# Kernel optimization log

Measured on AMD Instinct MI355X. Metric: run time of the kernel, lower is better.

Reference implementation:

```python
import jax, jax.numpy as jnp
import numpy as np

D_IN = 1024
D_OUT = 1024
B, S = 4, 4096


def setup_inputs() -> dict:
    key = jax.random.key(0)
    ks = jax.random.split(key, 7)
    scale = 1.0 / np.sqrt(D_IN)
    return {
        "x": jax.random.normal(ks[0], (B, S, D_IN), dtype=jnp.float32),
        "Wq": jax.random.uniform(ks[1], (D_IN, D_OUT), jnp.float32, -scale, scale),
        "bq": jax.random.uniform(ks[2], (D_OUT,), jnp.float32, -scale, scale),
        "Wk": jax.random.uniform(ks[3], (D_IN, D_OUT), jnp.float32, -scale, scale),
        "bk": jax.random.uniform(ks[4], (D_OUT,), jnp.float32, -scale, scale),
        "Wv": jax.random.uniform(ks[5], (D_IN, D_OUT), jnp.float32, -scale, scale),
        "bv": jax.random.uniform(ks[6], (D_OUT,), jnp.float32, -scale, scale),
    }


def reference(x, Wq, bq, Wk, bk, Wv, bv):
    # x: [B,S,d_in]
    q = jnp.einsum("bsd,de->bse", x, Wq) + bq  # [B,S,d_out]
    k = jnp.einsum("bsd,de->bse", x, Wk) + bk
    v = jnp.einsum("bsd,de->bse", x, Wv) + bv
    scores = jnp.einsum("bqe,bke->bqk", q, k) / jnp.sqrt(jnp.float32(D_OUT))  # [B,S,S]
    attn = jax.nn.softmax(scores, axis=2)
    return jnp.einsum("bqk,bke->bqe", attn, v)  # [B,S,d_out]
```

## Files before the change

### kernel.cpp

```cpp
#include <hip/hip_runtime.h>
#include <hip/hip_bf16.h>
#include <cstdint>

#define SEQ 4096
#define NB 4
#define DIM 1024
#define MTOT (NB * SEQ)
constexpr size_t EL = (size_t)MTOT * DIM;

using u16x8  = __attribute__((ext_vector_type(8))) unsigned short;
using bf16x8 = __attribute__((ext_vector_type(8))) __bf16;
using f32x4  = __attribute__((ext_vector_type(4))) float;

__device__ __forceinline__ unsigned short f2bf(float f) {
  return __builtin_bit_cast(unsigned short, __float2bfloat16(f));
}

__device__ __forceinline__ void gload16(const unsigned short* g, unsigned short* l) {
  __builtin_amdgcn_global_load_lds(
      (const __attribute__((address_space(1))) unsigned int*)g,
      (__attribute__((address_space(3))) unsigned int*)l, 16, 0, 0);
}
__device__ __forceinline__ void stage_half(const unsigned short* gsrc, size_t ld,
                                           unsigned short* ldst) {
  gload16(gsrc, ldst);
  gload16(gsrc + 64 * ld, ldst + 64 * 64);
}

#define BAR()   __builtin_amdgcn_s_barrier()
#define FENCE() asm volatile("" ::: "memory")

__global__ __launch_bounds__(256) void prep(const float* __restrict__ x,
                                            unsigned short* __restrict__ xb,
                                            const float* __restrict__ bq,
                                            const float* __restrict__ bk,
                                            const float* __restrict__ bv,
                                            float* __restrict__ bc,
                                            float* __restrict__ l) {
  const size_t gid = (size_t)blockIdx.x * 256 + threadIdx.x;
  const size_t i = gid * 4;
  float4 v = *(const float4*)(x + i);
  ushort4 o;
  o.x = f2bf(v.x); o.y = f2bf(v.y); o.z = f2bf(v.z); o.w = f2bf(v.w);
  *(ushort4*)(xb + i) = o;
  if (gid < MTOT) l[gid] = 0.f;
  if (gid < 3 * DIM)
    bc[gid] = gid < DIM ? bq[gid] : gid < 2 * DIM ? bk[gid - DIM] : bv[gid - 2 * DIM];
}

__global__ __launch_bounds__(256) void transpose_w3(const float* __restrict__ Wq,
                                                    const float* __restrict__ Wk,
                                                    const float* __restrict__ Wv,
                                                    unsigned short* __restrict__ WT) {
  const float* W = blockIdx.z == 0 ? Wq : blockIdx.z == 1 ? Wk : Wv;
  unsigned short* O = WT + (size_t)blockIdx.z * DIM * DIM;
  __shared__ float tile[32][33];
  const int tx = threadIdx.x, ty = threadIdx.y;
  const int d0 = blockIdx.y * 32, e0 = blockIdx.x * 32;
#pragma unroll
  for (int j = 0; j < 32; j += 8)
    tile[ty + j][tx] = W[(size_t)(d0 + ty + j) * DIM + e0 + tx];
  __syncthreads();
#pragma unroll
  for (int j = 0; j < 32; j += 8)
    O[(size_t)(e0 + ty + j) * DIM + d0 + tx] = f2bf(tile[tx][ty + j]);
}

enum { EPI_QKV = 0, EPI_EXP = 1, EPI_PV = 2 };

template <int EPI>
__device__ __forceinline__ void gemm_body(
    const unsigned short* __restrict__ A, const unsigned short* __restrict__ B,
    void* __restrict__ C, const float* __restrict__ bias, float* __restrict__ lsum,
    int K, int lda, int ldb, int ldc, float scale,
    int row0, int col0, int bz, long sA, long sB, long sC) {
  __shared__ unsigned short sm[2][2][256 * 64];
  const int t    = threadIdx.x;
  const int lane = t & 63;
  const int wave = t >> 6;
  const int wm   = wave >> 2;
  const int wn   = wave & 3;
  const int fr   = lane & 15;
  const int g    = lane >> 4;
  const int xr   = (fr & 7) << 4;

  const unsigned short* Ab = A + (size_t)bz * (size_t)sA;
  const unsigned short* Bb = B + (size_t)bz * (size_t)sB;

  const int srow = t >> 3;
  const int scol = ((((t & 7) << 4) ^ ((srow & 7) << 4)) >> 1);
  const unsigned short* gA = Ab + (size_t)(row0 + srow) * (size_t)lda + scol;
  const unsigned short* gB = Bb + (size_t)(col0 + srow) * (size_t)ldb + scol;

  const int arow = wm * 128 + fr;
  const int brow = wn * 64 + fr;
  const int c0 = (((g << 4)) ^ xr) >> 1;
  const int c1 = ((64 | (g << 4)) ^ xr) >> 1;

  f32x4 acc[8][4];
  const f32x4 z4 = {0.f, 0.f, 0.f, 0.f};
#pragma unroll
  for (int i = 0; i < 8; ++i)
#pragma unroll
    for (int j = 0; j < 4; ++j) acc[i][j] = z4;

  const int nt = K >> 6;

  stage_half(gA, lda, &sm[0][0][wave * 512]);
  stage_half(gA + 128 * (size_t)lda, lda, &sm[0][0][8192 + wave * 512]);
  stage_half(gB, ldb, &sm[0][1][wave * 512]);
  stage_half(gB + 128 * (size_t)ldb, ldb, &sm[0][1][8192 + wave * 512]);
  if (nt > 1) {
    stage_half(gB + 64, ldb, &sm[1][1][wave * 512]);
    stage_half(gB + 128 * (size_t)ldb + 64, ldb, &sm[1][1][8192 + wave * 512]);
    stage_half(gA + 64, lda, &sm[1][0][wave * 512]);
    asm volatile("s_waitcnt vmcnt(6)" ::: "memory");
  } else {
    asm volatile("s_waitcnt vmcnt(0)" ::: "memory");
  }
  BAR(); FENCE();

  bf16x8 a0[4][2], a1[4][2], b0[2][2], b1[2][2];

  for (int kt = 0; kt < nt; ++kt) {
    const int p = kt & 1;
    const unsigned short* As  = sm[p][0];
    const unsigned short* Bs2 = sm[p][1];

#pragma unroll
    for (int mi = 0; mi < 4; ++mi) {
      a0[mi][0] = *(const bf16x8*)(As + (arow + mi * 16) * 64 + c0);
      a0[mi][1] = *(const bf16x8*)(As + (arow + mi * 16) * 64 + c1);
    }
#pragma unroll
    for (int ni = 0; ni < 2; ++ni) {
      b0[ni][0] = *(const bf16x8*)(Bs2 + (brow + ni * 16) * 64 + c0);
      b0[ni][1] = *(const bf16x8*)(Bs2 + (brow + ni * 16) * 64 + c1);
    }
    if (kt + 1 < nt)
      stage_half(gA + 128 * (size_t)lda + (size_t)(kt + 1) * 64, lda,
                 &sm[p ^ 1][0][8192 + wave * 512]);
    FENCE(); BAR(); FENCE();
    __builtin_amdgcn_s_setprio(1);
#pragma unroll
    for (int mi = 0; mi < 4; ++mi)
#pragma unroll
      for (int ni = 0; ni < 2; ++ni) {
        acc[mi][ni] = __builtin_amdgcn_mfma_f32_16x16x32_bf16(a0[mi][0], b0[ni][0], acc[mi][ni], 0, 0, 0);
        acc[mi][ni] = __builtin_amdgcn_mfma_f32_16x16x32_bf16(a0[mi][1], b0[ni][1], acc[mi][ni], 0, 0, 0);
      }
    __builtin_amdgcn_s_setprio(0);
    FENCE(); BAR(); FENCE();

#pragma unroll
    for (int ni = 0; ni < 2; ++ni) {
      b1[ni][0] = *(const bf16x8*)(Bs2 + (brow + (ni + 2) * 16) * 64 + c0);
      b1[ni][1] = *(const bf16x8*)(Bs2 + (brow + (ni + 2) * 16) * 64 + c1);
    }
    FENCE(); BAR(); FENCE();
    __builtin_amdgcn_s_setprio(1);
#pragma unroll
    for (int mi = 0; mi < 4; ++mi)
#pragma unroll
      for (int ni = 0; ni < 2; ++ni) {
        acc[mi][ni + 2] = __builtin_amdgcn_mfma_f32_16x16x32_bf16(a0[mi][0], b1[ni][0], acc[mi][ni + 2], 0, 0, 0);
        acc[mi][ni + 2] = __builtin_amdgcn_mfma_f32_16x16x32_bf16(a0[mi][1], b1[ni][1], acc[mi][ni + 2], 0, 0, 0);
      }
    __builtin_amdgcn_s_setprio(0);
    FENCE(); BAR(); FENCE();

#pragma unroll
    for (int mi = 0; mi < 4; ++mi) {
      a1[mi][0] = *(const bf16x8*)(As + (arow + (mi + 4) * 16) * 64 + c0);
      a1[mi][1] = *(const bf16x8*)(As + (arow + (mi + 4) * 16) * 64 + c1);
    }
    if (kt + 2 < nt)
      stage_half(gB + (size_t)(kt + 2) * 64, ldb, &sm[p][1][wave * 512]);
    FENCE(); BAR(); FENCE();
    __builtin_amdgcn_s_setprio(1);
#pragma unroll
    for (int mi = 0; mi < 4; ++mi)
#pragma unroll
      for (int ni = 0; ni < 2; ++ni) {
        acc[mi + 4][ni] = __builtin_amdgcn_mfma_f32_16x16x32_bf16(a1[mi][0], b0[ni][0], acc[mi + 4][ni], 0, 0, 0);
        acc[mi + 4][ni] = __builtin_amdgcn_mfma_f32_16x16x32_bf16(a1[mi][1], b0[ni][1], acc[mi + 4][ni], 0, 0, 0);
      }
    __builtin_amdgcn_s_setprio(0);
    FENCE(); BAR(); FENCE();

    if (kt + 2 < nt) {
      stage_half(gB + 128 * (size_t)ldb + (size_t)(kt + 2) * 64, ldb,
                 &sm[p][1][8192 + wave * 512]);
      stage_half(gA + (size_t)(kt + 2) * 64, lda, &sm[p][0][wave * 512]);
      asm volatile("s_waitcnt vmcnt(6)" ::: "memory");
    } else {
      asm volatile("s_waitcnt vmcnt(0)" ::: "memory");
    }
    FENCE(); BAR(); FENCE();
    __builtin_amdgcn_s_setprio(1);
#pragma unroll
    for (int mi = 0; mi < 4; ++mi)
#pragma unroll
      for (int ni = 0; ni < 2; ++ni) {
        acc[mi + 4][ni + 2] = __builtin_amdgcn_mfma_f32_16x16x32_bf16(a1[mi][0], b1[ni][0], acc[mi + 4][ni + 2], 0, 0, 0);
        acc[mi + 4][ni + 2] = __builtin_amdgcn_mfma_f32_16x16x32_bf16(a1[mi][1], b1[ni][1], acc[mi + 4][ni + 2], 0, 0, 0);
      }
    __builtin_amdgcn_s_setprio(0);
    FENCE(); BAR(); FENCE();
  }

  char* Lb = (char*)&sm[0][0][0];
  const int rb = (lane >> 4) * 4;

  if constexpr (EPI == EPI_QKV) {
    const int which = col0 >> 10;
    const int lc0   = col0 & 1023;
    unsigned short* Co = (unsigned short*)C + (size_t)which * EL;
    if (which < 2) {
      float bb[4];
#pragma unroll
      for (int ni = 0; ni < 4; ++ni) bb[ni] = bias[col0 + wn * 64 + ni * 16 + fr];
#pragma unroll
      for (int mi = 0; mi < 8; ++mi) {
        const int r0 = wm * 128 + mi * 16 + rb;
#pragma unroll
        for (int ni = 0; ni < 4; ++ni) {
          const int c = wn * 64 + ni * 16 + fr;
#pragma unroll
          for (int j = 0; j < 4; ++j) {
            const int r = r0 + j;
            *(unsigned short*)(Lb + r * 512 + ((c * 2) ^ ((r & 7) << 4))) =
                f2bf(acc[mi][ni][j] + bb[ni]);
          }
        }
      }
      __syncthreads();
#pragma unroll 4
      for (int i = 0; i < 16; ++i) {
        const int G = i * 512 + t;
        const int r = G >> 5, c16 = G & 31;
        u16x8 v = *(const u16x8*)(Lb + r * 512 + ((c16 * 16) ^ ((r & 7) << 4)));
        *(u16x8*)(Co + (size_t)(row0 + r) * DIM + lc0 + c16 * 8) = v;
      }
    } else {
#pragma unroll
      for (int ni = 0; ni < 4; ++ni) {
        const int c = wn * 64 + ni * 16 + fr;
        const float bb = bias[col0 + c];
#pragma unroll
        for (int mi = 0; mi < 8; ++mi) {
          const int r0 = wm * 128 + mi * 16 + rb;
          ushort4 pk;
          pk.x = f2bf(acc[mi][ni][0] + bb);
          pk.y = f2bf(acc[mi][ni][1] + bb);
          pk.z = f2bf(acc[mi][ni][2] + bb);
          pk.w = f2bf(acc[mi][ni][3] + bb);
          *(ushort4*)(Lb + c * 512 + ((r0 * 2) ^ ((c & 7) << 4))) = pk;
        }
      }
      __syncthreads();
#pragma unroll 4
      for (int i = 0; i < 16; ++i) {
        const int G = i * 512 + t;
        const int e = G >> 5, m16 = G & 31;
        u16x8 v = *(const u16x8*)(Lb + e * 512 + ((m16 * 16) ^ ((e & 7) << 4)));
        *(u16x8*)(Co + (size_t)(lc0 + e) * MTOT + row0 + m16 * 8) = v;
      }
    }
  } else if constexpr (EPI == EPI_EXP) {
#pragma unroll
    for (int mi = 0; mi < 8; ++mi)
#pragma unroll
      for (int ni = 0; ni < 4; ++ni)
#pragma unroll
        for (int j = 0; j < 4; ++j)
          acc[mi][ni][j] = exp2f(acc[mi][ni][j] * scale);

#pragma unroll
    for (int mi = 0; mi < 8; ++mi)
#pragma unroll
      for (int j = 0; j < 4; ++j) {
        float s = acc[mi][0][j] + acc[mi][1][j] + acc[mi][2][j] + acc[mi][3][j];
        s += __shfl_xor(s, 1);
        s += __shfl_xor(s, 2);
        s += __shfl_xor(s, 4);
        s += __shfl_xor(s, 8);
        if (fr == 0)
          atomicAdd(&lsum[(size_t)bz * SEQ + row0 + wm * 128 + mi * 16 + rb + j], s);
      }

#pragma unroll
    for (int mi = 0; mi < 8; ++mi) {
      const int r0 = wm * 128 + mi * 16 + rb;
#pragma unroll
      for (int ni = 0; ni < 4; ++ni) {
        const int c = wn * 64 + ni * 16 + fr;
#pragma unroll
        for (int j = 0; j < 4; ++j) {
          const int r = r0 + j;
          *(unsigned short*)(Lb + r * 512 + ((c * 2) ^ ((r & 7) << 4))) =
              f2bf(acc[mi][ni][j]);
        }
      }
    }
    __syncthreads();
    unsigned short* Co = (unsigned short*)C + (size_t)bz * (size_t)sC;
#pragma unroll 4
    for (int i = 0; i < 16; ++i) {
      const int G = i * 512 + t;
      const int r = G >> 5, c16 = G & 31;
      u16x8 v = *(const u16x8*)(Lb + r * 512 + ((c16 * 16) ^ ((r & 7) << 4)));
      *(u16x8*)(Co + (size_t)(row0 + r) * (size_t)ldc + col0 + c16 * 8) = v;
    }
  } else {
    float* Co = (float*)C + (size_t)bz * (size_t)sC;
#pragma unroll
    for (int h = 0; h < 2; ++h) {
      if (h) __syncthreads();
      if (wm == h) {
#pragma unroll
        for (int mi = 0; mi < 8; ++mi) {
          const int r0 = mi * 16 + rb;
#pragma unroll
          for (int ni = 0; ni < 4; ++ni) {
            const int c = wn * 64 + ni * 16 + fr;
#pragma unroll
            for (int j = 0; j < 4; ++j) {
              const int r = r0 + j;
              *(float*)(Lb + r * 1024 + ((c * 4) ^ ((r & 7) << 4))) = acc[mi][ni][j];
            }
          }
        }
      }
      __syncthreads();
#pragma unroll 4
      for (int i = 0; i < 16; ++i) {
        const int G = i * 512 + t;
        const int r = G >> 6, c4 = G & 63;
        f32x4 v = *(const f32x4*)(Lb + r * 1024 + ((c4 * 16) ^ ((r & 7) << 4)));
        const size_t grow = (size_t)row0 + h * 128 + r;
        const float inv = 1.0f / lsum[(size_t)bz * SEQ + grow];
        v *= inv;
        *(f32x4*)(Co + grow * (size_t)ldc + col0 + c4 * 4) = v;
      }
    }
  }
}


__global__ __launch_bounds__(512, 2) void gemm_qkv(
    const unsigned short* __restrict__ A, const unsigned short* __restrict__ B,
    unsigned short* __restrict__ C, const float* __restrict__ bcat) {
  const int flat = (int)blockIdx.x + 64 * (int)blockIdx.y;
  const int xcd = flat & 7, j = flat >> 3;
  const int row = xcd * 8 + (j & 7);
  const int col = j >> 3;
  gemm_body<EPI_QKV>(A, B, C, bcat, nullptr, DIM, DIM, DIM, DIM, 1.f,
                     row * 256, col * 256, 0, 0, 0, 0);
}

__global__ __launch_bounds__(512, 2) void gemm_exp(
    const unsigned short* __restrict__ A, const unsigned short* __restrict__ B,
    unsigned short* __restrict__ C, float* __restrict__ lsum) {
  const int flat = (int)blockIdx.x +
                   (int)gridDim.x * ((int)blockIdx.y + (int)gridDim.y * (int)blockIdx.z);
  const int xcd = flat & 7, j = flat >> 3;
  const int bz  = (xcd >> 2) * 2 + (j >> 6);
  const int jj  = j & 63;
  const int row = (xcd & 3) * 4 + (jj & 3);
  const int col = jj >> 2;
  gemm_body<EPI_EXP>(A, B, C, nullptr, lsum, DIM, DIM, DIM, SEQ, 0.04508422f,
                     row * 256, col * 256, bz,
                     (long)SEQ * DIM, (long)SEQ * DIM, (long)SEQ * SEQ);
}

__global__ __launch_bounds__(512, 2) void gemm_pv(
    const unsigned short* __restrict__ A, const unsigned short* __restrict__ B,
    float* __restrict__ C, float* __restrict__ lsum) {
  const int flat = (int)blockIdx.x +
                   (int)gridDim.x * ((int)blockIdx.y + (int)gridDim.y * (int)blockIdx.z);
  const int nf  = (flat & 7) * 32 + (flat >> 3);
  const int b   = nf >> 6;
  const int rc  = nf & 63;
  const int row = rc >> 2, col = rc & 3;
  gemm_body<EPI_PV>(A, B, C, nullptr, lsum, SEQ, SEQ, MTOT, DIM, 1.f,
                    row * 256, col * 256, b,
                    (long)SEQ * SEQ, (long)SEQ, (long)SEQ * DIM);
}

extern "C" void kernel_launch(void* const* d_in, const int* in_sizes, int n_in,
                              void* d_out, int out_size, void* d_ws, size_t ws_size,
                              hipStream_t stream) {
  (void)in_sizes; (void)n_in; (void)out_size; (void)ws_size;
  const float* x  = (const float*)d_in[0];
  const float* Wq = (const float*)d_in[1];
  const float* bq = (const float*)d_in[2];
  const float* Wk = (const float*)d_in[3];
  const float* bk = (const float*)d_in[4];
  const float* Wv = (const float*)d_in[5];
  const float* bv = (const float*)d_in[6];
  float* out = (float*)d_out;

  const size_t SALL = (size_t)NB * SEQ * SEQ;
  unsigned short* Q  = (unsigned short*)d_ws;
  unsigned short* Km = Q + EL;
  unsigned short* VT = Km + EL;
  unsigned short* Sb = VT + EL;
  unsigned short* WT = Sb + SALL;
  float*          l  = (float*)(WT + (size_t)3 * DIM * DIM);
  float*          bc = l + MTOT;
  unsigned short* xb = Sb;

  prep<<<dim3(EL / 1024), dim3(256), 0, stream>>>(x, xb, bq, bk, bv, bc, l);
  transpose_w3<<<dim3(32, 32, 3), dim3(32, 8), 0, stream>>>(Wq, Wk, Wv, WT);

  gemm_qkv<<<dim3(64, 12), 512, 0, stream>>>(xb, WT, Q, bc);

  gemm_exp<<<dim3(SEQ / 256, SEQ / 256, NB), 512, 0, stream>>>(Q, Km, Sb, l);

  gemm_pv<<<dim3(DIM / 256, SEQ / 256, NB), 512, 0, stream>>>(Sb, VT, out, l);
}
```

Measured before the change: 401.5 us.

## Fold the K projection into a precomputed Wq·Wkᵀ matrix to skip the K GEMM

Result: slower. 432.0 us (+7.6%).

```diff
diff --git a/kernel.cpp b/kernel.cpp
--- a/kernel.cpp
+++ b/kernel.cpp
@@ -16,7 +16,7 @@
   return __builtin_bit_cast(unsigned short, __float2bfloat16(f));
 }
 
-__device__ __forceinline__ void gload16(const unsigned short* g, unsigned short* l) {
+__device__ __forceinline__ void gload16(const void* g, void* l) {
   __builtin_amdgcn_global_load_lds(
       (const __attribute__((address_space(1))) unsigned int*)g,
       (__attribute__((address_space(3))) unsigned int*)l, 16, 0, 0);
@@ -30,30 +30,53 @@
 #define BAR()   __builtin_amdgcn_s_barrier()
 #define FENCE() asm volatile("" ::: "memory")
 
+
+#define NXB ((int)(EL / 1024))
 __global__ __launch_bounds__(256) void prep(const float* __restrict__ x,
                                             unsigned short* __restrict__ xb,
-                                            const float* __restrict__ bq,
-                                            const float* __restrict__ bk,
+                                            const float* __restrict__ Wq,
+                                            const float* __restrict__ Wk,
+                                            unsigned short* __restrict__ Wq_b,
+                                            unsigned short* __restrict__ Wk_b,
                                             const float* __restrict__ bv,
                                             float* __restrict__ bc,
                                             float* __restrict__ l) {
-  const size_t gid = (size_t)blockIdx.x * 256 + threadIdx.x;
-  const size_t i = gid * 4;
-  float4 v = *(const float4*)(x + i);
-  ushort4 o;
-  o.x = f2bf(v.x); o.y = f2bf(v.y); o.z = f2bf(v.z); o.w = f2bf(v.w);
-  *(ushort4*)(xb + i) = o;
-  if (gid < MTOT) l[gid] = 0.f;
-  if (gid < 3 * DIM)
-    bc[gid] = gid < DIM ? bq[gid] : gid < 2 * DIM ? bk[gid - DIM] : bv[gid - 2 * DIM];
-}
-
-__global__ __launch_bounds__(256) void transpose_w3(const float* __restrict__ Wq,
-                                                    const float* __restrict__ Wk,
-                                                    const float* __restrict__ Wv,
-                                                    unsigned short* __restrict__ WT) {
-  const float* W = blockIdx.z == 0 ? Wq : blockIdx.z == 1 ? Wk : Wv;
-  unsigned short* O = WT + (size_t)blockIdx.z * DIM * DIM;
+  const int bid = (int)blockIdx.x;
+  const int t = threadIdx.x;
+  if (bid < NXB) {
+    const size_t gid = (size_t)bid * 256 + t;
+    const size_t i = gid * 4;
+    float4 v = *(const float4*)(x + i);
+    ushort4 o;
+    o.x = f2bf(v.x); o.y = f2bf(v.y); o.z = f2bf(v.z); o.w = f2bf(v.w);
+    *(ushort4*)(xb + i) = o;
+    if (gid < MTOT) l[gid] = 0.f;
+    if (gid < 2 * DIM) bc[gid] = gid < DIM ? 0.f : bv[gid - DIM];
+  } else {
+    const int wb = bid - NXB;
+    const int z = wb >> 10;
+    const float* W = z ? Wk : Wq;
+    unsigned short* O = z ? Wk_b : Wq_b;
+    const size_t i = ((size_t)(wb & 1023) * 1024) + (size_t)t * 4;
+    float4 v = *(const float4*)(W + i);
+    ushort4 o;
+    o.x = f2bf(v.x); o.y = f2bf(v.y); o.z = f2bf(v.z); o.w = f2bf(v.w);
+    *(ushort4*)(O + i) = o;
+  }
+}
+
+__global__ __launch_bounds__(256) void bias_proj(const float* __restrict__ bq,
+                                                 const float* __restrict__ Wk,
+                                                 float* __restrict__ bc) {
+  const int e = blockIdx.x * 256 + threadIdx.x;
+  float s = 0.f;
+#pragma unroll 4
+  for (int d = 0; d < DIM; ++d) s += bq[d] * Wk[(size_t)e * DIM + d];
+  bc[e] = s;
+}
+
+__global__ __launch_bounds__(256) void transpose_w(const float* __restrict__ W,
+                                                   unsigned short* __restrict__ WT) {
   __shared__ float tile[32][33];
   const int tx = threadIdx.x, ty = threadIdx.y;
   const int d0 = blockIdx.y * 32, e0 = blockIdx.x * 32;
@@ -63,7 +86,72 @@
   __syncthreads();
 #pragma unroll
   for (int j = 0; j < 32; j += 8)
-    O[(size_t)(e0 + ty + j) * DIM + d0 + tx] = f2bf(tile[tx][ty + j]);
+    WT[(size_t)(e0 + ty + j) * DIM + d0 + tx] = f2bf(tile[tx][ty + j]);
+}
+
+__global__ __launch_bounds__(256) void gemm_mt(
+    const unsigned short* __restrict__ A, const unsigned short* __restrict__ B,
+    unsigned short* __restrict__ C) {
+  __shared__ unsigned short As[128 * 32];
+  __shared__ unsigned short Bs[128 * 32];
+  const int t = threadIdx.x;
+  const int lane = t & 63;
+  const int wave = t >> 6;
+  const size_t row0 = (size_t)blockIdx.x * 128;
+  const size_t col0 = (size_t)blockIdx.y * 128;
+  const int wm = (wave >> 1) * 64;
+  const int wn = (wave & 1) * 64;
+  const int fr = lane & 15;
+  const int fk = (lane >> 4) * 8;
+
+  f32x4 acc[4][4];
+  const f32x4 z4 = {0.f, 0.f, 0.f, 0.f};
+#pragma unroll
+  for (int i = 0; i < 4; ++i)
+#pragma unroll
+    for (int j = 0; j < 4; ++j) acc[i][j] = z4;
+
+  const int srow = t >> 2;
+  const int sseg = (t & 3) * 8;
+  const unsigned short* gA = A + (row0 + srow) * (size_t)DIM + sseg;
+  const unsigned short* gB = B + (col0 + srow) * (size_t)DIM + sseg;
+  unsigned short* lA = As + wave * 512;
+  unsigned short* lB = Bs + wave * 512;
+  const size_t a64 = (size_t)64 * DIM;
+
+  for (int k0 = 0; k0 < DIM; k0 += 32) {
+    gload16(gA + k0, lA);
+    gload16(gA + k0 + a64, lA + 2048);
+    gload16(gB + k0, lB);
+    gload16(gB + k0 + a64, lB + 2048);
+    __syncthreads();
+    bf16x8 af[4], bfr[4];
+#pragma unroll
+    for (int mi = 0; mi < 4; ++mi)
+      af[mi] = *(const bf16x8*)(As + (wm + mi * 16 + fr) * 32 + fk);
+#pragma unroll
+    for (int ni = 0; ni < 4; ++ni)
+      bfr[ni] = *(const bf16x8*)(Bs + (wn + ni * 16 + fr) * 32 + fk);
+#pragma unroll
+    for (int mi = 0; mi < 4; ++mi)
+#pragma unroll
+      for (int ni = 0; ni < 4; ++ni)
+        acc[mi][ni] = __builtin_amdgcn_mfma_f32_16x16x32_bf16(af[mi], bfr[ni], acc[mi][ni], 0, 0, 0);
+    __syncthreads();
+  }
+
+  const int rb = (lane >> 4) * 4;
+#pragma unroll
+  for (int ni = 0; ni < 4; ++ni) {
+    size_t gc = col0 + wn + ni * 16 + fr;
+#pragma unroll
+    for (int mi = 0; mi < 4; ++mi) {
+      size_t gr = row0 + wm + mi * 16 + rb;
+#pragma unroll
+      for (int j = 0; j < 4; ++j)
+        C[(gr + j) * (size_t)DIM + gc] = f2bf(acc[mi][ni][j]);
+    }
+  }
 }
 
 enum { EPI_QKV = 0, EPI_EXP = 1, EPI_PV = 2 };
@@ -216,7 +304,7 @@
     const int which = col0 >> 10;
     const int lc0   = col0 & 1023;
     unsigned short* Co = (unsigned short*)C + (size_t)which * EL;
-    if (which < 2) {
+    if (which < 1) {
       float bb[4];
 #pragma unroll
       for (int ni = 0; ni < 4; ++ni) bb[ni] = bias[col0 + wn * 64 + ni * 16 + fr];
@@ -346,7 +434,6 @@
     }
   }
 }
-
 
 __global__ __launch_bounds__(512, 2) void gemm_qkv(
     const unsigned short* __restrict__ A, const unsigned short* __restrict__ B,
@@ -396,27 +483,31 @@
   const float* Wq = (const float*)d_in[1];
   const float* bq = (const float*)d_in[2];
   const float* Wk = (const float*)d_in[3];
-  const float* bk = (const float*)d_in[4];
   const float* Wv = (const float*)d_in[5];
   const float* bv = (const float*)d_in[6];
   float* out = (float*)d_out;
 
   const size_t SALL = (size_t)NB * SEQ * SEQ;
-  unsigned short* Q  = (unsigned short*)d_ws;
-  unsigned short* Km = Q + EL;
-  unsigned short* VT = Km + EL;
-  unsigned short* Sb = VT + EL;
-  unsigned short* WT = Sb + SALL;
-  float*          l  = (float*)(WT + (size_t)3 * DIM * DIM);
-  float*          bc = l + MTOT;
-  unsigned short* xb = Sb;
-
-  prep<<<dim3(EL / 1024), dim3(256), 0, stream>>>(x, xb, bq, bk, bv, bc, l);
-  transpose_w3<<<dim3(32, 32, 3), dim3(32, 8), 0, stream>>>(Wq, Wk, Wv, WT);
-
-  gemm_qkv<<<dim3(64, 12), 512, 0, stream>>>(xb, WT, Q, bc);
-
-  gemm_exp<<<dim3(SEQ / 256, SEQ / 256, NB), 512, 0, stream>>>(Q, Km, Sb, l);
-
-  gemm_pv<<<dim3(DIM / 256, SEQ / 256, NB), 512, 0, stream>>>(Sb, VT, out, l);
-}
+  unsigned short* Q    = (unsigned short*)d_ws;
+  unsigned short* VT   = Q + EL;
+  unsigned short* xb   = VT + EL;
+  unsigned short* Sb   = xb + EL;
+  unsigned short* MT   = Sb;
+  unsigned short* WvT  = MT + (size_t)DIM * DIM;
+  unsigned short* Wq_b = WvT + (size_t)DIM * DIM;
+  unsigned short* Wk_b = Wq_b + (size_t)DIM * DIM;
+  float*          l    = (float*)(Sb + SALL);
+  float*          bc   = l + MTOT;
+
+  prep<<<dim3(NXB + 2048), dim3(256), 0, stream>>>(x, xb, Wq, Wk, Wq_b, Wk_b,
+                                                   bv, bc, l);
+  transpose_w<<<dim3(32, 32), dim3(32, 8), 0, stream>>>(Wv, WvT);
+  bias_proj<<<dim3(4), dim3(256), 0, stream>>>(bq, Wk, bc);
+  gemm_mt<<<dim3(8, 8), 256, 0, stream>>>(Wk_b, Wq_b, MT);
+
+  gemm_qkv<<<dim3(64, 8), 512, 0, stream>>>(xb, MT, Q, bc);
+
+  gemm_exp<<<dim3(SEQ / 256, SEQ / 256, NB), 512, 0, stream>>>(Q, xb, Sb, l);
+
+  gemm_pv<<<dim3(4, 16, 4), 512, 0, stream>>>(Sb, VT, out, l);
+}
```
